# Optimization experiments

Measured on AMD Instinct MI355X. Metric: run time of the kernel, lower is better.

## Reference

```python
import jax, jax.numpy as jnp
import numpy as np

B, IH, IW = 16, 32, 32
N = IH * IW
HEADS, DIM_HEAD = 8, 64
INNER = HEADS * DIM_HEAD  # 512
INP, OUP = 512, 512
SCALE = DIM_HEAD ** -0.5


def _relative_index():
    # replicate torch.meshgrid (ij) -> coords [2, N]
    yy, xx = np.meshgrid(np.arange(IH), np.arange(IW), indexing='ij')
    coords = np.stack([yy.reshape(-1), xx.reshape(-1)])  # [2, N]
    rel = coords[:, :, None] - coords[:, None, :]        # [2, N, N]
    rel[0] += IH - 1
    rel[1] += IW - 1
    rel[0] *= 2 * IW - 1
    return jnp.asarray(rel.sum(0).reshape(-1), dtype=jnp.int32)  # [N*N]


def setup_inputs() -> dict:
    key = jax.random.key(0)
    k1, k2, k3, k4, k5 = jax.random.split(key, 5)
    x = jax.random.normal(k1, (B, N, INP), dtype=jnp.float32)
    W_qkv = jax.random.normal(k2, (INP, 3 * INNER), dtype=jnp.float32) * (INP ** -0.5)
    # table is initialized to zeros in the module; use small randn so bias path is exercised
    rel_table = jax.random.normal(k3, ((2 * IH - 1) * (2 * IW - 1), HEADS), dtype=jnp.float32) * 0.02
    W_out = jax.random.normal(k4, (INNER, OUP), dtype=jnp.float32) * (INNER ** -0.5)
    b_out = jax.random.normal(k5, (OUP,), dtype=jnp.float32) * 0.02
    return {
        'x': x,
        'W_qkv': W_qkv,
        'rel_table': rel_table,
        'W_out': W_out,
        'b_out': b_out,
        'rel_index': _relative_index(),
    }


def reference(x, W_qkv, rel_table, W_out, b_out, rel_index):
    b, n, _ = x.shape
    qkv = x @ W_qkv                                            # [b, n, 3*inner]
    q, k, v = jnp.split(qkv, 3, axis=-1)
    def to_heads(t):
        return t.reshape(b, n, HEADS, DIM_HEAD).transpose(0, 2, 1, 3)  # [b, h, n, d]
    q, k, v = to_heads(q), to_heads(k), to_heads(v)
    dots = jnp.einsum('bhnd,bhmd->bhnm', q, k) * SCALE         # [b, h, n, n]
    bias = rel_table[rel_index].reshape(n, n, HEADS).transpose(2, 0, 1)[None]  # [1, h, n, n]
    attn = jax.nn.softmax(dots + bias, axis=-1)
    out = jnp.einsum('bhnm,bhmd->bhnd', attn, v)               # [b, h, n, d]
    out = out.transpose(0, 2, 1, 3).reshape(b, n, INNER)       # [b, n, inner]
    return out @ W_out + b_out
```

## Files before the change

### kernel.cpp

```cpp
#include <hip/hip_runtime.h>
#include <math.h>

#define BATCH 16
#define NTOK 1024
#define HEADS 8
#define DHEAD 64
#define INNER 512
#define QKV_COLS 1536
#define SCALE_L2E 0.1803368801111244f
#define LOG2E 1.4426950408889634f

#if __has_builtin(__builtin_amdgcn_exp2f)
#define EXP2F(x) __builtin_amdgcn_exp2f(x)
#else
#define EXP2F(x) __expf((x) * 0.6931471805599453f)
#endif

typedef _Float16 f16x8 __attribute__((ext_vector_type(8)));
typedef _Float16 f16x4 __attribute__((ext_vector_type(4)));
typedef float f32x4 __attribute__((ext_vector_type(4)));

#define MFMA32(a, b, c) __builtin_amdgcn_mfma_f32_16x16x32_f16(a, b, c, 0, 0, 0)

__device__ __forceinline__ void glds16(const void* g, void* l) {
    __builtin_amdgcn_global_load_lds(
        (const __attribute__((address_space(1))) unsigned int*)g,
        (__attribute__((address_space(3))) unsigned int*)l, 16, 0, 0);
}

#define XV (BATCH * NTOK * INNER / 4)
#define XB (XV / 256)
#define WQTILES 192
#define WOTILES 64

__global__ __launch_bounds__(256)
void convert_inputs(const float* __restrict__ x, const float* __restrict__ Wq,
                    const float* __restrict__ Wo, _Float16* __restrict__ x_h,
                    _Float16* __restrict__ Wq_t, _Float16* __restrict__ Wo_t) {
    const int b = blockIdx.x, t = threadIdx.x;
    if (b < XB) {
        const int idx = b * 256 + t;
        float4 v = ((const float4*)x)[idx];
        f16x4 h;
        h[0] = (_Float16)v.x; h[1] = (_Float16)v.y;
        h[2] = (_Float16)v.z; h[3] = (_Float16)v.w;
        *(f16x4*)(x_h + (size_t)idx * 4) = h;
        return;
    }
    const bool isQ = (b < XB + WQTILES);
    const int b2  = isQ ? (b - XB) : (b - XB - WQTILES);
    const int ntl = isQ ? 24 : 8;
    const int ldw = isQ ? QKV_COLS : INNER;
    const float*   W  = isQ ? Wq   : Wo;
    _Float16*      Wt = isQ ? Wq_t : Wo_t;
    const int k0 = (b2 / ntl) * 64, n0 = (b2 % ntl) * 64;
    const int kk = k0 + (t >> 4) * 4, nn = n0 + (t & 15) * 4;
    f32x4 v0 = *(const f32x4*)(W + (size_t)(kk + 0) * ldw + nn);
    f32x4 v1 = *(const f32x4*)(W + (size_t)(kk + 1) * ldw + nn);
    f32x4 v2 = *(const f32x4*)(W + (size_t)(kk + 2) * ldw + nn);
    f32x4 v3 = *(const f32x4*)(W + (size_t)(kk + 3) * ldw + nn);
#pragma unroll
    for (int f = 0; f < 4; ++f) {
        f16x4 h;
        h[0] = (_Float16)v0[f]; h[1] = (_Float16)v1[f];
        h[2] = (_Float16)v2[f]; h[3] = (_Float16)v3[f];
        *(f16x4*)(Wt + (size_t)(nn + f) * INNER + kk) = h;
    }
}

template<int MODE>
__global__ __launch_bounds__(256, 3)
void gemm_f16(const _Float16* __restrict__ A, const _Float16* __restrict__ Bt,
              const float* __restrict__ bias, void* __restrict__ Cout,
              _Float16* __restrict__ vtg, int M, int N, int K) {
    __shared__ _Float16 As[3][128 * 32];
    __shared__ _Float16 Bs[3][128 * 32];

    const int t    = threadIdx.x;
    const int l    = t & 63;
    const int w    = t >> 6;
    const int wm   = w >> 1;
    const int wn   = w & 1;
    const int quad = l >> 4;
    const int lrow = l & 15;

    const int nwg = gridDim.x * gridDim.y;
    int bid = blockIdx.x + gridDim.x * blockIdx.y;
    bid = (bid & 7) * (nwg >> 3) + (bid >> 3);
    const size_t row0 = (size_t)(bid / gridDim.x) * 128;
    const size_t col0 = (size_t)(bid % gridDim.x) * 128;

    const int srow = t >> 2;
    const int sch  = t & 3;

    f32x4 acc[4][4] = {};
    const int NSTEP = K >> 5;

    auto stage = [&](int kk, int bufi) {
#pragma unroll
        for (int p = 0; p < 2; ++p) {
            const int r  = p * 64 + srow;
            const int gc = (sch ^ ((r >> 1) & 3)) * 8;
            glds16(A  + (row0 + r) * K + kk * 32 + gc, (char*)As[bufi] + p * 4096 + t * 16);
            glds16(Bt + (col0 + r) * K + kk * 32 + gc, (char*)Bs[bufi] + p * 4096 + t * 16);
        }
    };

    stage(0, 0);
    stage(1, 1);

    int buf = 0, pre = 2;
    for (int kk = 0; kk < NSTEP; ++kk) {
        if (kk + 1 < NSTEP) asm volatile("s_waitcnt vmcnt(4)" ::: "memory");
        else                asm volatile("s_waitcnt vmcnt(0)" ::: "memory");
        __builtin_amdgcn_s_barrier();
        __builtin_amdgcn_sched_barrier(0);
        if (kk + 2 < NSTEP) stage(kk + 2, pre);

        f16x8 af[4], bf[4];
#pragma unroll
        for (int i = 0; i < 4; ++i) {
            const int r = wm * 64 + i * 16 + lrow;
            af[i] = *(const f16x8*)(As[buf] + r * 32 + ((quad ^ ((r >> 1) & 3)) * 8));
        }
#pragma unroll
        for (int j = 0; j < 4; ++j) {
            const int r = wn * 64 + j * 16 + lrow;
            bf[j] = *(const f16x8*)(Bs[buf] + r * 32 + ((quad ^ ((r >> 1) & 3)) * 8));
        }
#pragma unroll
        for (int i = 0; i < 4; ++i)
#pragma unroll
            for (int j = 0; j < 4; ++j)
                acc[i][j] = MFMA32(bf[j], af[i], acc[i][j]);

        buf = (buf == 2) ? 0 : buf + 1;
        pre = (pre == 2) ? 0 : pre + 1;
    }

    const bool isV = (MODE == 2) && (col0 >= 2 * INNER);
#pragma unroll
    for (int i = 0; i < 4; ++i) {
        const size_t m = row0 + wm * 64 + i * 16 + lrow;
#pragma unroll
        for (int j = 0; j < 4; ++j) {
            const size_t c = col0 + wn * 64 + j * 16 + quad * 4;
            f32x4 v = acc[i][j];
            if (MODE == 0) {
                float4 bv = *(const float4*)(bias + c);
                v[0] += bv.x; v[1] += bv.y; v[2] += bv.z; v[3] += bv.w;
                *(f32x4*)((float*)Cout + m * N + c) = v;
            } else if (!isV) {
                f16x4 hv;
                hv[0] = (_Float16)v[0]; hv[1] = (_Float16)v[1];
                hv[2] = (_Float16)v[2]; hv[3] = (_Float16)v[3];
                *(f16x4*)((_Float16*)Cout + m * N + c) = hv;
            } else {
                const int cv = (int)(c - 2 * INNER);
                const int hh = cv >> 6, db = cv & 63;
                const size_t vb = (((size_t)(m >> 10) * HEADS + hh) * 64 + db) * NTOK
                                  + (m & (NTOK - 1));
#pragma unroll
                for (int reg = 0; reg < 4; ++reg)
                    vtg[vb + (size_t)reg * NTOK] = (_Float16)v[reg];
            }
        }
    }
}

__global__ __launch_bounds__(512, 4)
void attn_f16_v8(const _Float16* __restrict__ qkv, const _Float16* __restrict__ vt,
                 const float* __restrict__ rel_table, _Float16* __restrict__ out) {
    __shared__ _Float16 Ks[3][64 * 64];
    __shared__ _Float16 Vs[3][64 * 64];
    __shared__ float biasS[3969];

    const int t    = threadIdx.x;
    const int l    = t & 63;
    const int w    = t >> 6;
    const int quad = l >> 4;
    const int lrow = l & 15;
    const int h    = blockIdx.y;
    const int bb   = blockIdx.z;
    const int qr0  = blockIdx.x * 256 + w * 32;

    for (int idx = t; idx < 3969; idx += 512)
        biasS[idx] = rel_table[idx * HEADS + h] * LOG2E;

    const size_t tokbase = (size_t)bb * NTOK;

    f16x8 aq[2][2];
#pragma unroll
    for (int mt = 0; mt < 2; ++mt)
#pragma unroll
        for (int ksi = 0; ksi < 2; ++ksi)
            aq[mt][ksi] = *(const f16x8*)(qkv + (tokbase + qr0 + mt * 16 + lrow) * QKV_COLS
                                          + h * DHEAD + ksi * 32 + quad * 8);

    f32x4 O[2][4] = {};
    float l0 = 0.f, l1 = 0.f;

    const int iy = qr0 >> 5;
    const int krow_base = 8 * (lrow >> 2) + (lrow & 3);
    const int fKl = (lrow & 3) + 4 * ((lrow >> 2) & 1);

    const int kr  = t >> 3;
    const int ksl = t & 7;
    const int fKr = (kr & 3) + 4 * ((kr >> 3) & 1);
    const _Float16* kbase = qkv + tokbase * QKV_COLS + INNER + h * DHEAD;
    const _Float16* vbase = vt + ((size_t)(bb * HEADS + h) * 64) * NTOK;

    auto stage = [&](int jt, int bufi) {
        const int j0s = jt * 64;
        glds16(kbase + (size_t)(j0s + kr) * QKV_COLS + (ksl ^ fKr) * 8, (char*)Ks[bufi] + t * 16);
        glds16(vbase + (size_t)kr * NTOK + j0s + (ksl ^ (kr & 7)) * 8,  (char*)Vs[bufi] + t * 16);
    };

    stage(0, 0);
    stage(1, 1);
    asm volatile("s_waitcnt lgkmcnt(0)" ::: "memory");

    int buf = 0, pre = 2;
    for (int jt = 0; jt < 16; ++jt) {
        if (jt < 15) asm volatile("s_waitcnt vmcnt(2)" ::: "memory");
        else         asm volatile("s_waitcnt vmcnt(0)" ::: "memory");
        __builtin_amdgcn_s_barrier();
        __builtin_amdgcn_sched_barrier(0);
        if (jt + 2 < 16) stage(jt + 2, pre);

#pragma unroll
        for (int jn0 = 0; jn0 < 2; ++jn0) {
            f16x8 pb0, pb1;
#pragma unroll
            for (int s = 0; s < 2; ++s) {
                const int krow = jn0 * 32 + krow_base + 4 * s;
                f32x4 S0 = {}, S1 = {};
                __builtin_amdgcn_s_setprio(1);
#pragma unroll
                for (int ksi = 0; ksi < 2; ++ksi) {
                    f16x8 bk = *(const f16x8*)(Ks[buf] + krow * 64
                                               + (((ksi * 4 + quad) ^ fKl) * 8));
                    S0 = MFMA32(bk, aq[0][ksi], S0);
                    S1 = MFMA32(bk, aq[1][ksi], S1);
                }
                __builtin_amdgcn_s_setprio(0);
                const int base = (iy - (jt * 2 + jn0) + 31) * 63 + 31 + lrow
                                 - 8 * quad - 4 * s;
                {
                    float p0 = EXP2F(fmaf(S0[0], SCALE_L2E, biasS[base - 0]));
                    float p1 = EXP2F(fmaf(S0[1], SCALE_L2E, biasS[base - 1]));
                    float p2 = EXP2F(fmaf(S0[2], SCALE_L2E, biasS[base - 2]));
                    float p3 = EXP2F(fmaf(S0[3], SCALE_L2E, biasS[base - 3]));
                    l0 += (p0 + p1) + (p2 + p3);
                    pb0[s * 4 + 0] = (_Float16)p0; pb0[s * 4 + 1] = (_Float16)p1;
                    pb0[s * 4 + 2] = (_Float16)p2; pb0[s * 4 + 3] = (_Float16)p3;
                }
                {
                    const int b1 = base + 16;
                    float p0 = EXP2F(fmaf(S1[0], SCALE_L2E, biasS[b1 - 0]));
                    float p1 = EXP2F(fmaf(S1[1], SCALE_L2E, biasS[b1 - 1]));
                    float p2 = EXP2F(fmaf(S1[2], SCALE_L2E, biasS[b1 - 2]));
                    float p3 = EXP2F(fmaf(S1[3], SCALE_L2E, biasS[b1 - 3]));
                    l1 += (p0 + p1) + (p2 + p3);
                    pb1[s * 4 + 0] = (_Float16)p0; pb1[s * 4 + 1] = (_Float16)p1;
                    pb1[s * 4 + 2] = (_Float16)p2; pb1[s * 4 + 3] = (_Float16)p3;
                }
            }

            __builtin_amdgcn_s_setprio(1);
#pragma unroll
            for (int dn = 0; dn < 4; ++dn) {
                const int d = dn * 16 + lrow;
                f16x8 av = *(const f16x8*)(Vs[buf] + d * 64
                              + (((jn0 * 4 + quad) ^ (d & 7)) * 8));
                O[0][dn] = MFMA32(av, pb0, O[0][dn]);
                O[1][dn] = MFMA32(av, pb1, O[1][dn]);
            }
            __builtin_amdgcn_s_setprio(0);
        }

        buf = (buf == 2) ? 0 : buf + 1;
        pre = (pre == 2) ? 0 : pre + 1;
    }

#pragma unroll
    for (int mt = 0; mt < 2; ++mt) {
        float s = mt ? l1 : l0;
        s += __shfl_xor(s, 16);
        s += __shfl_xor(s, 32);
        const float inv = 1.f / s;
        const size_t orow = (tokbase + qr0 + mt * 16 + lrow) * INNER + h * DHEAD;
#pragma unroll
        for (int dn = 0; dn < 4; ++dn) {
            const f32x4 o = O[mt][dn];
            f16x4 ov;
            ov[0] = (_Float16)(o[0] * inv); ov[1] = (_Float16)(o[1] * inv);
            ov[2] = (_Float16)(o[2] * inv); ov[3] = (_Float16)(o[3] * inv);
            *(f16x4*)(out + orow + dn * 16 + quad * 4) = ov;
        }
    }
}

extern "C" void kernel_launch(void* const* d_in, const int* in_sizes, int n_in,
                              void* d_out, int out_size, void* d_ws, size_t ws_size,
                              hipStream_t stream) {
    const float* x         = (const float*)d_in[0];
    const float* W_qkv     = (const float*)d_in[1];
    const float* rel_table = (const float*)d_in[2];
    const float* W_out     = (const float*)d_in[3];
    const float* b_out     = (const float*)d_in[4];

    _Float16* x_h   = (_Float16*)d_ws;
    _Float16* Wq_t  = x_h + (size_t)BATCH * NTOK * INNER;
    _Float16* Wo_t  = Wq_t + (size_t)INNER * QKV_COLS;
    _Float16* qkv_h = Wo_t + (size_t)INNER * INNER;
    _Float16* att_h = qkv_h + (size_t)BATCH * NTOK * QKV_COLS;
    _Float16* vt_g  = att_h + (size_t)BATCH * NTOK * INNER;

    const int M = BATCH * NTOK;

    convert_inputs<<<XB + WQTILES + WOTILES, 256, 0, stream>>>(
        x, W_qkv, W_out, x_h, Wq_t, Wo_t);

    gemm_f16<2><<<dim3(QKV_COLS / 128, M / 128), 256, 0, stream>>>(
        x_h, Wq_t, nullptr, qkv_h, vt_g, M, QKV_COLS, INNER);

    attn_f16_v8<<<dim3(NTOK / 256, HEADS, BATCH), 512, 0, stream>>>(
        qkv_h, vt_g, rel_table, att_h);

    gemm_f16<0><<<dim3(INNER / 128, M / 128), 256, 0, stream>>>(
        att_h, Wo_t, b_out, d_out, nullptr, M, INNER, INNER);
}
```

Baseline: 205.9 us.

## Software-pipeline PV MFMA one tile behind QK and trim bias LDS window

The attention kernel now computes the S=QK^T and exp for tile jt while doing the P·V MFMAs for tile jt-1, keeping the previous P fragments in registers. This lets exp/VALU work overlap with matrix ops. K/V buffering goes from 3 to 4 stages, since V of the prior tile must stay live while two tiles are prefetched. The bias table load is cut to just the 39 rows this block needs, which reduces LDS fill work and footprint. The cost is extra registers for the carried P fragments and more LDS for the fourth buffer, which may reduce occupancy.

After: 210.1 us. 2.1% more time.

```diff
diff --git a/kernel.cpp b/kernel.cpp
--- a/kernel.cpp
+++ b/kernel.cpp
@@ -169,11 +169,11 @@
 }
 
 __global__ __launch_bounds__(512, 4)
-void attn_f16_v8(const _Float16* __restrict__ qkv, const _Float16* __restrict__ vt,
+void attn_f16_v9(const _Float16* __restrict__ qkv, const _Float16* __restrict__ vt,
                  const float* __restrict__ rel_table, _Float16* __restrict__ out) {
-    __shared__ _Float16 Ks[3][64 * 64];
-    __shared__ _Float16 Vs[3][64 * 64];
-    __shared__ float biasS[3969];
+    __shared__ _Float16 Ks[4][64 * 64];
+    __shared__ _Float16 Vs[4][64 * 64];
+    __shared__ float biasS[39 * 63];
 
     const int t    = threadIdx.x;
     const int l    = t & 63;
@@ -183,9 +183,12 @@
     const int h    = blockIdx.y;
     const int bb   = blockIdx.z;
     const int qr0  = blockIdx.x * 256 + w * 32;
-
-    for (int idx = t; idx < 3969; idx += 512)
-        biasS[idx] = rel_table[idx * HEADS + h] * LOG2E;
+    const int B8   = blockIdx.x * 8;
+
+    for (int idx = t; idx < 39 * 63; idx += 512) {
+        const int rr = idx / 63, cc = idx - rr * 63;
+        biasS[idx] = rel_table[((B8 + rr) * 63 + cc) * HEADS + h] * LOG2E;
+    }
 
     const size_t tokbase = (size_t)bb * NTOK;
 
@@ -200,9 +203,9 @@
     f32x4 O[2][4] = {};
     float l0 = 0.f, l1 = 0.f;
 
-    const int iy = qr0 >> 5;
     const int krow_base = 8 * (lrow >> 2) + (lrow & 3);
     const int fKl = (lrow & 3) + 4 * ((lrow >> 2) & 1);
+    const int cpre = 31 + lrow - 8 * quad;
 
     const int kr  = t >> 3;
     const int ksl = t & 7;
@@ -210,27 +213,31 @@
     const _Float16* kbase = qkv + tokbase * QKV_COLS + INNER + h * DHEAD;
     const _Float16* vbase = vt + ((size_t)(bb * HEADS + h) * 64) * NTOK;
 
-    auto stage = [&](int jt, int bufi) {
+    auto stage = [&](int jt) {
+        const int bufi = jt & 3;
         const int j0s = jt * 64;
         glds16(kbase + (size_t)(j0s + kr) * QKV_COLS + (ksl ^ fKr) * 8, (char*)Ks[bufi] + t * 16);
         glds16(vbase + (size_t)kr * NTOK + j0s + (ksl ^ (kr & 7)) * 8,  (char*)Vs[bufi] + t * 16);
     };
 
-    stage(0, 0);
-    stage(1, 1);
+    stage(0);
+    stage(1);
     asm volatile("s_waitcnt lgkmcnt(0)" ::: "memory");
 
-    int buf = 0, pre = 2;
+    f16x8 pp00, pp01, pp10, pp11;
+
     for (int jt = 0; jt < 16; ++jt) {
         if (jt < 15) asm volatile("s_waitcnt vmcnt(2)" ::: "memory");
         else         asm volatile("s_waitcnt vmcnt(0)" ::: "memory");
         __builtin_amdgcn_s_barrier();
         __builtin_amdgcn_sched_barrier(0);
-        if (jt + 2 < 16) stage(jt + 2, pre);
+        if (jt + 2 < 16) stage(jt + 2);
+
+        const int kb = jt & 3;
+        f16x8 pn00, pn01, pn10, pn11;
 
 #pragma unroll
         for (int jn0 = 0; jn0 < 2; ++jn0) {
-            f16x8 pb0, pb1;
 #pragma unroll
             for (int s = 0; s < 2; ++s) {
                 const int krow = jn0 * 32 + krow_base + 4 * s;
@@ -238,22 +245,26 @@
                 __builtin_amdgcn_s_setprio(1);
 #pragma unroll
                 for (int ksi = 0; ksi < 2; ++ksi) {
-                    f16x8 bk = *(const f16x8*)(Ks[buf] + krow * 64
+                    f16x8 bk = *(const f16x8*)(Ks[kb] + krow * 64
                                                + (((ksi * 4 + quad) ^ fKl) * 8));
                     S0 = MFMA32(bk, aq[0][ksi], S0);
                     S1 = MFMA32(bk, aq[1][ksi], S1);
                 }
                 __builtin_amdgcn_s_setprio(0);
-                const int base = (iy - (jt * 2 + jn0) + 31) * 63 + 31 + lrow
-                                 - 8 * quad - 4 * s;
+                const int base = (w - (jt * 2 + jn0) + 31) * 63 + cpre - 4 * s;
                 {
                     float p0 = EXP2F(fmaf(S0[0], SCALE_L2E, biasS[base - 0]));
                     float p1 = EXP2F(fmaf(S0[1], SCALE_L2E, biasS[base - 1]));
                     float p2 = EXP2F(fmaf(S0[2], SCALE_L2E, biasS[base - 2]));
                     float p3 = EXP2F(fmaf(S0[3], SCALE_L2E, biasS[base - 3]));
                     l0 += (p0 + p1) + (p2 + p3);
-                    pb0[s * 4 + 0] = (_Float16)p0; pb0[s * 4 + 1] = (_Float16)p1;
-                    pb0[s * 4 + 2] = (_Float16)p2; pb0[s * 4 + 3] = (_Float16)p3;
+                    if (jn0 == 0) {
+                        pn00[s * 4 + 0] = (_Float16)p0; pn00[s * 4 + 1] = (_Float16)p1;
+                        pn00[s * 4 + 2] = (_Float16)p2; pn00[s * 4 + 3] = (_Float16)p3;
+                    } else {
+                        pn10[s * 4 + 0] = (_Float16)p0; pn10[s * 4 + 1] = (_Float16)p1;
+                        pn10[s * 4 + 2] = (_Float16)p2; pn10[s * 4 + 3] = (_Float16)p3;
+                    }
                 }
                 {
                     const int b1 = base + 16;
@@ -262,25 +273,50 @@
                     float p2 = EXP2F(fmaf(S1[2], SCALE_L2E, biasS[b1 - 2]));
                     float p3 = EXP2F(fmaf(S1[3], SCALE_L2E, biasS[b1 - 3]));
                     l1 += (p0 + p1) + (p2 + p3);
-                    pb1[s * 4 + 0] = (_Float16)p0; pb1[s * 4 + 1] = (_Float16)p1;
-                    pb1[s * 4 + 2] = (_Float16)p2; pb1[s * 4 + 3] = (_Float16)p3;
+                    if (jn0 == 0) {
+                        pn01[s * 4 + 0] = (_Float16)p0; pn01[s * 4 + 1] = (_Float16)p1;
+                        pn01[s * 4 + 2] = (_Float16)p2; pn01[s * 4 + 3] = (_Float16)p3;
+                    } else {
+                        pn11[s * 4 + 0] = (_Float16)p0; pn11[s * 4 + 1] = (_Float16)p1;
+                        pn11[s * 4 + 2] = (_Float16)p2; pn11[s * 4 + 3] = (_Float16)p3;
+                    }
                 }
             }
-
+        }
+
+        if (jt > 0) {
+            const int vb = (jt - 1) & 3;
             __builtin_amdgcn_s_setprio(1);
 #pragma unroll
             for (int dn = 0; dn < 4; ++dn) {
                 const int d = dn * 16 + lrow;
-                f16x8 av = *(const f16x8*)(Vs[buf] + d * 64
-                              + (((jn0 * 4 + quad) ^ (d & 7)) * 8));
-                O[0][dn] = MFMA32(av, pb0, O[0][dn]);
-                O[1][dn] = MFMA32(av, pb1, O[1][dn]);
+                f16x8 av0 = *(const f16x8*)(Vs[vb] + d * 64 + (((0 + quad) ^ (d & 7)) * 8));
+                O[0][dn] = MFMA32(av0, pp00, O[0][dn]);
+                O[1][dn] = MFMA32(av0, pp01, O[1][dn]);
+                f16x8 av1 = *(const f16x8*)(Vs[vb] + d * 64 + (((4 + quad) ^ (d & 7)) * 8));
+                O[0][dn] = MFMA32(av1, pp10, O[0][dn]);
+                O[1][dn] = MFMA32(av1, pp11, O[1][dn]);
             }
             __builtin_amdgcn_s_setprio(0);
         }
 
-        buf = (buf == 2) ? 0 : buf + 1;
-        pre = (pre == 2) ? 0 : pre + 1;
+        pp00 = pn00; pp01 = pn01; pp10 = pn10; pp11 = pn11;
+    }
+
+    {
+        const int vb = 15 & 3;
+        __builtin_amdgcn_s_setprio(1);
+#pragma unroll
+        for (int dn = 0; dn < 4; ++dn) {
+            const int d = dn * 16 + lrow;
+            f16x8 av0 = *(const f16x8*)(Vs[vb] + d * 64 + (((0 + quad) ^ (d & 7)) * 8));
+            O[0][dn] = MFMA32(av0, pp00, O[0][dn]);
+            O[1][dn] = MFMA32(av0, pp01, O[1][dn]);
+            f16x8 av1 = *(const f16x8*)(Vs[vb] + d * 64 + (((4 + quad) ^ (d & 7)) * 8));
+            O[0][dn] = MFMA32(av1, pp10, O[0][dn]);
+            O[1][dn] = MFMA32(av1, pp11, O[1][dn]);
+        }
+        __builtin_amdgcn_s_setprio(0);
     }
 
 #pragma unroll
@@ -325,7 +361,7 @@
     gemm_f16<2><<<dim3(QKV_COLS / 128, M / 128), 256, 0, stream>>>(
         x_h, Wq_t, nullptr, qkv_h, vt_g, M, QKV_COLS, INNER);
 
-    attn_f16_v8<<<dim3(NTOK / 256, HEADS, BATCH), 512, 0, stream>>>(
+    attn_f16_v9<<<dim3(NTOK / 256, HEADS, BATCH), 512, 0, stream>>>(
         qkv_h, vt_g, rel_table, att_h);
 
     gemm_f16<0><<<dim3(INNER / 128, M / 128), 256, 0, stream>>>(
```
